# Kernel optimization log

Hardware: AMD Instinct MI355X
Metric: run time of the kernel (lower is better)

The kernel has to match this reference:

```python
import jax, jax.numpy as jnp
import numpy as np

MEM_DIM = 2000
FEA_DIM = 256
SHRINK_THRES = 0.0025
EPS = 1e-06


def setup_inputs() -> dict:
    key = jax.random.key(0)
    k1, k2 = jax.random.split(key)
    x = jax.random.normal(k1, (65536, FEA_DIM), dtype=jnp.float32)
    stdv = 1.0 / np.sqrt(FEA_DIM)
    weight = jax.random.uniform(k2, (MEM_DIM, FEA_DIM), dtype=jnp.float32,
                                minval=-stdv, maxval=stdv)
    temperature = jnp.asarray(0.5, dtype=jnp.float32)
    return {"input": x, "weight": weight, "temperature": temperature}


def hard_shrink_relu(a, lambd=SHRINK_THRES, epsilon=EPS):
    a = jnp.clip(a, -10.0, 10.0)
    denom = jnp.maximum(jnp.abs(a - lambd) + epsilon, epsilon)
    out = jax.nn.relu(a - lambd) * a / denom
    return jnp.where(jnp.isnan(out) | jnp.isinf(out), 0.0, out)


def reference(input, weight, temperature):
    mem_dim = weight.shape[0]
    inv_m = 1.0 / mem_dim
    x = jnp.clip(input, -10.0, 10.0)                      # [N, F]
    att = jnp.einsum('nf,mf->nm', x, weight)              # [N, M]
    att = jax.nn.softmax(att / temperature, axis=1)
    # shrink_thres > 0 branch
    att = hard_shrink_relu(att)
    weight_sum = jnp.sum(att, axis=1, keepdims=True)      # [N, 1]
    zero_mask = weight_sum < 1e-08
    att = att / (weight_sum + 1e-08)
    att = jnp.where(zero_mask, inv_m, att)                # rows with ~zero sum -> uniform
    att = jnp.where(jnp.isnan(att) | jnp.isinf(att), inv_m, att)
    output = jnp.einsum('nm,mf->nf', att, weight)         # [N, F]
    return output, att
```

## Files before the change

kernel.cpp:

```cpp
#include <hip/hip_runtime.h>
#include <hip/hip_bf16.h>
#include <cstdint>

#define N_ROWS 65536
#define FEA    256
#define MEM    2000
#define MEMP   2048
#define LAMBD  0.0025f
#define SEPS   1e-6f
#define NW     16

typedef __attribute__((ext_vector_type(8))) _Float16 f16x8;
typedef __attribute__((ext_vector_type(8))) short    bf16x8;
typedef __attribute__((ext_vector_type(4))) float    f32x4;

__device__ __forceinline__ short f2bf(float f) {
    union { float f; uint32_t u; } v; v.f = f;
    uint32_t r = v.u + 0x7fffu + ((v.u >> 16) & 1u);
    return (short)(r >> 16);
}

__global__ __launch_bounds__(256) void prep_kernel(const float* __restrict__ W,
                                                   _Float16* __restrict__ Whl2,
                                                   short* __restrict__ Wt) {
    __shared__ float tile[8][260];
    const int t  = threadIdx.x;
    const int m0 = blockIdx.x * 8;
    const int row = t >> 5, col = (t & 31) * 8;
    const int m = m0 + row;
    if (m < MEM) {
        f32x4 a = *(const f32x4*)(W + (size_t)m * FEA + col);
        f32x4 b = *(const f32x4*)(W + (size_t)m * FEA + col + 4);
        #pragma unroll
        for (int u = 0; u < 4; ++u) { tile[row][col+u] = a[u]; tile[row][col+4+u] = b[u]; }
    } else {
        #pragma unroll
        for (int u = 0; u < 8; ++u) tile[row][col+u] = 0.f;
    }
    __syncthreads();
    {
        const int c = col >> 5, q = (col >> 3) & 3;
        const int tt = m >> 4, lr = m & 15;
        _Float16 hi[8], lo[8];
        #pragma unroll
        for (int j = 0; j < 8; ++j) {
            float w = tile[row][col + j];
            _Float16 h = (_Float16)w;
            hi[j] = h;
            lo[j] = (_Float16)((w - (float)h) * 2048.0f);
        }
        _Float16* dst = Whl2 + (((size_t)(tt * 8 + c)) << 10) + (q * 16 + lr) * 16;
        *(f16x8*)dst       = *(f16x8*)&hi[0];
        *(f16x8*)(dst + 8) = *(f16x8*)&lo[0];
    }
    {
        short buf[8];
        #pragma unroll
        for (int j = 0; j < 8; ++j) buf[j] = f2bf(tile[j][t]);
        *(bf16x8*)(Wt + (size_t)t * MEMP + m0) = *(bf16x8*)&buf[0];
    }
}

__global__ __launch_bounds__(1024, 4) void score_kernel(const float* __restrict__ x,
                                                        const _Float16* __restrict__ Whl2,
                                                        const float* __restrict__ temp,
                                                        float* __restrict__ att) {
    __shared__ __align__(16) _Float16 ah_s[32][264];
    __shared__ __align__(16) _Float16 al_s[32][264];
    __shared__ float redbuf[NW][32];
    __shared__ float redglob[32];

    const int tid  = threadIdx.x;
    const int lane = tid & 63;
    const int wid  = tid >> 6;
    const int lr   = lane & 15;
    const int q    = lane >> 4;
    const size_t r0 = (size_t)blockIdx.x * 32;
    const float invT = 1.0f / temp[0];

    {
        const int srow = tid >> 5, scol = (tid & 31) * 8;
        const float* xp = x + (r0 + srow) * FEA + scol;
        f32x4 v0 = *(const f32x4*)xp;
        f32x4 v1 = *(const f32x4*)(xp + 4);
        #pragma unroll
        for (int w = 0; w < 4; ++w) {
            float f0 = fminf(fmaxf(v0[w], -10.f), 10.f);
            float f1 = fminf(fmaxf(v1[w], -10.f), 10.f);
            _Float16 h0 = (_Float16)f0, h1 = (_Float16)f1;
            ah_s[srow][scol + w]     = h0;
            ah_s[srow][scol + 4 + w] = h1;
            al_s[srow][scol + w]     = (_Float16)((f0 - (float)h0) * 2048.0f);
            al_s[srow][scol + 4 + w] = (_Float16)((f1 - (float)h1) * 2048.0f);
        }
    }
    __syncthreads();

    f32x4 acc[2][8];
    #pragma unroll
    for (int rg = 0; rg < 2; ++rg)
        #pragma unroll
        for (int jj = 0; jj < 8; ++jj) acc[rg][jj] = (f32x4){0.f, 0.f, 0.f, 0.f};

    #pragma unroll 1
    for (int c = 0; c < 8; ++c) {
        f16x8 ah[2], al[2];
        #pragma unroll
        for (int rg = 0; rg < 2; ++rg) {
            ah[rg] = *(const f16x8*)&ah_s[rg * 16 + lr][c * 32 + q * 8];
            al[rg] = *(const f16x8*)&al_s[rg * 16 + lr][c * 32 + q * 8];
        }
        #pragma unroll
        for (int jj = 0; jj < 8; ++jj) {
            const int t = wid + 16 * jj;
            const _Float16* bp = Whl2 + (((size_t)(t * 8 + c)) << 10) + lane * 16;
            f16x8 bh = *(const f16x8*)bp;
            f16x8 bl = *(const f16x8*)(bp + 8);
            #pragma unroll
            for (int rg = 0; rg < 2; ++rg) {
                f32x4 z = (f32x4){0.f, 0.f, 0.f, 0.f};
                f32x4 t1 = __builtin_amdgcn_mfma_f32_16x16x32_f16(al[rg], bh, z, 0, 0, 0);
                t1 = __builtin_amdgcn_mfma_f32_16x16x32_f16(ah[rg], bl, t1, 0, 0, 0);
                acc[rg][jj] = __builtin_amdgcn_mfma_f32_16x16x32_f16(ah[rg], bh, acc[rg][jj], 0, 0, 0);
                acc[rg][jj] += t1 * (1.0f / 2048.0f);
            }
        }
    }

    const bool lastv = (wid < 13);

    auto xred = [&](float v[2][4], bool ismax) {
        #pragma unroll
        for (int m = 1; m < 16; m <<= 1)
            #pragma unroll
            for (int rg = 0; rg < 2; ++rg)
                #pragma unroll
                for (int i = 0; i < 4; ++i) {
                    float o = __shfl_xor(v[rg][i], m, 64);
                    v[rg][i] = ismax ? fmaxf(v[rg][i], o) : (v[rg][i] + o);
                }
        if (lr == 0) {
            #pragma unroll
            for (int rg = 0; rg < 2; ++rg)
                #pragma unroll
                for (int i = 0; i < 4; ++i) redbuf[wid][rg * 16 + q * 4 + i] = v[rg][i];
        }
        __syncthreads();
        if (tid < 32) {
            float r = redbuf[0][tid];
            #pragma unroll
            for (int w = 1; w < NW; ++w) {
                float o = redbuf[w][tid];
                r = ismax ? fmaxf(r, o) : (r + o);
            }
            redglob[tid] = r;
        }
        __syncthreads();
        #pragma unroll
        for (int rg = 0; rg < 2; ++rg)
            #pragma unroll
            for (int i = 0; i < 4; ++i) v[rg][i] = redglob[rg * 16 + q * 4 + i];
        __syncthreads();
    };

    float M[2][4];
    #pragma unroll
    for (int rg = 0; rg < 2; ++rg)
        #pragma unroll
        for (int i = 0; i < 4; ++i) M[rg][i] = -3.0e38f;
    #pragma unroll
    for (int jj = 0; jj < 8; ++jj) {
        if (jj < 7 || lastv) {
            #pragma unroll
            for (int rg = 0; rg < 2; ++rg)
                #pragma unroll
                for (int i = 0; i < 4; ++i) M[rg][i] = fmaxf(M[rg][i], acc[rg][jj][i]);
        }
    }
    xred(M, true);

    #pragma unroll
    for (int jj = 0; jj < 8; ++jj) {
        const bool v = (jj < 7) || lastv;
        #pragma unroll
        for (int rg = 0; rg < 2; ++rg)
            #pragma unroll
            for (int i = 0; i < 4; ++i)
                acc[rg][jj][i] = v ? __expf((acc[rg][jj][i] - M[rg][i]) * invT) : 0.0f;
    }

    float Z[2][4];
    #pragma unroll
    for (int rg = 0; rg < 2; ++rg)
        #pragma unroll
        for (int i = 0; i < 4; ++i) Z[rg][i] = 0.f;
    #pragma unroll
    for (int jj = 0; jj < 8; ++jj)
        #pragma unroll
        for (int rg = 0; rg < 2; ++rg)
            #pragma unroll
            for (int i = 0; i < 4; ++i) Z[rg][i] += acc[rg][jj][i];
    xred(Z, false);

    #pragma unroll
    for (int rg = 0; rg < 2; ++rg)
        #pragma unroll
        for (int i = 0; i < 4; ++i) Z[rg][i] = 1.0f / Z[rg][i];
    #pragma unroll
    for (int jj = 0; jj < 8; ++jj)
        #pragma unroll
        for (int rg = 0; rg < 2; ++rg)
            #pragma unroll
            for (int i = 0; i < 4; ++i) {
                float a = acc[rg][jj][i] * Z[rg][i];
                float d = a - LAMBD;
                acc[rg][jj][i] = (d > 0.f) ? (d * a) / (d + SEPS) : 0.f;
            }

    float WS[2][4];
    #pragma unroll
    for (int rg = 0; rg < 2; ++rg)
        #pragma unroll
        for (int i = 0; i < 4; ++i) WS[rg][i] = 0.f;
    #pragma unroll
    for (int jj = 0; jj < 8; ++jj)
        #pragma unroll
        for (int rg = 0; rg < 2; ++rg)
            #pragma unroll
            for (int i = 0; i < 4; ++i) WS[rg][i] += acc[rg][jj][i];
    xred(WS, false);

    const float inv_m = 1.0f / (float)MEM;
    float scl[2][4];
    bool  zr[2][4];
    #pragma unroll
    for (int rg = 0; rg < 2; ++rg)
        #pragma unroll
        for (int i = 0; i < 4; ++i) {
            scl[rg][i] = 1.0f / (WS[rg][i] + 1e-8f);
            zr[rg][i]  = (WS[rg][i] < 1e-8f);
        }

    #pragma unroll
    for (int jj = 0; jj < 8; ++jj) {
        if (jj < 7 || lastv) {
            const int mcol = (wid + 16 * jj) * 16 + lr;
            #pragma unroll
            for (int rg = 0; rg < 2; ++rg)
                #pragma unroll
                for (int i = 0; i < 4; ++i) {
                    float vv = zr[rg][i] ? inv_m : acc[rg][jj][i] * scl[rg][i];
                    att[(r0 + rg * 16 + q * 4 + i) * (size_t)MEM + mcol] = vv;
                }
        }
    }
}

__global__ __launch_bounds__(512) void gemm2_kernel(const float* __restrict__ att,
                                                    const short* __restrict__ Wt,
                                                    float* __restrict__ out) {
    __shared__ short Asm[2][128][40];
    __shared__ short Bsm[2][256][40];
    const int tid  = threadIdx.x;
    const int lane = tid & 63;
    const int wid  = tid >> 6;
    const int rg   = wid >> 2;
    const int cg   = wid & 3;
    const int lr   = lane & 15;
    const int lk   = (lane >> 4) * 8;
    const size_t r0 = (size_t)blockIdx.x * 128;

    const int sa_row = tid >> 2, sa_ko = (tid & 3) * 8;
    const int sb_f   = tid >> 1, sb_ko = (tid & 1) * 16;

    auto stage = [&](int buf, int kc) {
        const int k0 = kc * 32;
        {
            int k = k0 + sa_ko;
            short b[8];
            if (k < MEM) {
                const float* ap = att + (r0 + sa_row) * (size_t)MEM + k;
                f32x4 v0 = *(const f32x4*)ap;
                f32x4 v1 = *(const f32x4*)(ap + 4);
                #pragma unroll
                for (int u = 0; u < 4; ++u) { b[u] = f2bf(v0[u]); b[4+u] = f2bf(v1[u]); }
            } else {
                #pragma unroll
                for (int u = 0; u < 8; ++u) b[u] = 0;
            }
            *(bf16x8*)&Asm[buf][sa_row][sa_ko] = *(bf16x8*)&b[0];
        }
        {
            const short* wp = Wt + (size_t)sb_f * MEMP + k0 + sb_ko;
            bf16x8 b0 = *(const bf16x8*)wp;
            bf16x8 b1 = *(const bf16x8*)(wp + 8);
            *(bf16x8*)&Bsm[buf][sb_f][sb_ko]     = b0;
            *(bf16x8*)&Bsm[buf][sb_f][sb_ko + 8] = b1;
        }
    };

    f32x4 acc[4][4];
    #pragma unroll
    for (int i = 0; i < 4; ++i)
        #pragma unroll
        for (int j = 0; j < 4; ++j) acc[i][j] = (f32x4){0.f, 0.f, 0.f, 0.f};

    stage(0, 0);
    int cur = 0;
    for (int kc = 0; kc < 63; ++kc) {
        __syncthreads();
        if (kc + 1 < 63) stage(cur ^ 1, kc + 1);
        bf16x8 a_[4], b_[4];
        #pragma unroll
        for (int i = 0; i < 4; ++i) a_[i] = *(const bf16x8*)&Asm[cur][rg * 64 + i * 16 + lr][lk];
        #pragma unroll
        for (int j = 0; j < 4; ++j) b_[j] = *(const bf16x8*)&Bsm[cur][cg * 64 + j * 16 + lr][lk];
        #pragma unroll
        for (int i = 0; i < 4; ++i)
            #pragma unroll
            for (int j = 0; j < 4; ++j)
                acc[i][j] = __builtin_amdgcn_mfma_f32_16x16x32_bf16(a_[i], b_[j], acc[i][j], 0, 0, 0);
        cur ^= 1;
    }

    #pragma unroll
    for (int i = 0; i < 4; ++i)
        #pragma unroll
        for (int j = 0; j < 4; ++j)
            #pragma unroll
            for (int ii = 0; ii < 4; ++ii) {
                size_t row = r0 + rg * 64 + i * 16 + (lane >> 4) * 4 + ii;
                out[row * FEA + cg * 64 + j * 16 + lr] = acc[i][j][ii];
            }
}

extern "C" void kernel_launch(void* const* d_in, const int* in_sizes, int n_in,
                              void* d_out, int out_size, void* d_ws, size_t ws_size,
                              hipStream_t stream) {
    const float* x = (const float*)d_in[0];
    const float* W = (const float*)d_in[1];
    const float* T = (const float*)d_in[2];
    float* out = (float*)d_out;
    float* att = out + (size_t)N_ROWS * FEA;
    _Float16* Whl2 = (_Float16*)d_ws;
    short*    Wt   = (short*)((char*)d_ws + (2u << 20));

    prep_kernel<<<dim3(256), dim3(256), 0, stream>>>(W, Whl2, Wt);
    score_kernel<<<dim3(N_ROWS / 32), dim3(1024), 0, stream>>>(x, Whl2, T, att);
    gemm2_kernel<<<dim3(N_ROWS / 128), dim3(512), 0, stream>>>(att, Wt, out);
}
```

Baseline: 559.7 us.

## Fold temperature into weights, reorder score MFMA loops, use fast reciprocals

Temperature scaling moves into the weight preparation kernel, so the scores come out already divided by temperature and the softmax subtract-multiply is dropped. The score GEMM loop is swapped to iterate over output tiles outermost with K innermost, keeping separate hi and lo-correction accumulators. This removes the per-step vector add and scale and the zero-init MFMA chain, but LDS A fragments are now reloaded for each tile. Exact divisions are replaced with hardware rcp approximations, and att stores are regrouped by row.

New measurement: 1.289 ms. +130.2%, slower.

```diff
diff --git a/kernel.cpp b/kernel.cpp
--- a/kernel.cpp
+++ b/kernel.cpp
@@ -21,6 +21,7 @@
 }
 
 __global__ __launch_bounds__(256) void prep_kernel(const float* __restrict__ W,
+                                                   const float* __restrict__ temp,
                                                    _Float16* __restrict__ Whl2,
                                                    short* __restrict__ Wt) {
     __shared__ float tile[8][260];
@@ -28,6 +29,7 @@
     const int m0 = blockIdx.x * 8;
     const int row = t >> 5, col = (t & 31) * 8;
     const int m = m0 + row;
+    const float invT = 1.0f / temp[0];
     if (m < MEM) {
         f32x4 a = *(const f32x4*)(W + (size_t)m * FEA + col);
         f32x4 b = *(const f32x4*)(W + (size_t)m * FEA + col + 4);
@@ -44,7 +46,7 @@
         _Float16 hi[8], lo[8];
         #pragma unroll
         for (int j = 0; j < 8; ++j) {
-            float w = tile[row][col + j];
+            float w = tile[row][col + j] * invT;
             _Float16 h = (_Float16)w;
             hi[j] = h;
             lo[j] = (_Float16)((w - (float)h) * 2048.0f);
@@ -63,7 +65,6 @@
 
 __global__ __launch_bounds__(1024, 4) void score_kernel(const float* __restrict__ x,
                                                         const _Float16* __restrict__ Whl2,
-                                                        const float* __restrict__ temp,
                                                         float* __restrict__ att) {
     __shared__ __align__(16) _Float16 ah_s[32][264];
     __shared__ __align__(16) _Float16 al_s[32][264];
@@ -76,7 +77,6 @@
     const int lr   = lane & 15;
     const int q    = lane >> 4;
     const size_t r0 = (size_t)blockIdx.x * 32;
-    const float invT = 1.0f / temp[0];
 
     {
         const int srow = tid >> 5, scol = (tid & 31) * 8;
@@ -97,34 +97,30 @@
     __syncthreads();
 
     f32x4 acc[2][8];
-    #pragma unroll
-    for (int rg = 0; rg < 2; ++rg)
-        #pragma unroll
-        for (int jj = 0; jj < 8; ++jj) acc[rg][jj] = (f32x4){0.f, 0.f, 0.f, 0.f};
 
     #pragma unroll 1
-    for (int c = 0; c < 8; ++c) {
-        f16x8 ah[2], al[2];
-        #pragma unroll
-        for (int rg = 0; rg < 2; ++rg) {
-            ah[rg] = *(const f16x8*)&ah_s[rg * 16 + lr][c * 32 + q * 8];
-            al[rg] = *(const f16x8*)&al_s[rg * 16 + lr][c * 32 + q * 8];
-        }
-        #pragma unroll
-        for (int jj = 0; jj < 8; ++jj) {
-            const int t = wid + 16 * jj;
-            const _Float16* bp = Whl2 + (((size_t)(t * 8 + c)) << 10) + lane * 16;
-            f16x8 bh = *(const f16x8*)bp;
-            f16x8 bl = *(const f16x8*)(bp + 8);
-            #pragma unroll
-            for (int rg = 0; rg < 2; ++rg) {
-                f32x4 z = (f32x4){0.f, 0.f, 0.f, 0.f};
-                f32x4 t1 = __builtin_amdgcn_mfma_f32_16x16x32_f16(al[rg], bh, z, 0, 0, 0);
-                t1 = __builtin_amdgcn_mfma_f32_16x16x32_f16(ah[rg], bl, t1, 0, 0, 0);
-                acc[rg][jj] = __builtin_amdgcn_mfma_f32_16x16x32_f16(ah[rg], bh, acc[rg][jj], 0, 0, 0);
-                acc[rg][jj] += t1 * (1.0f / 2048.0f);
-            }
-        }
+    for (int jj = 0; jj < 8; ++jj) {
+        const int t = wid + 16 * jj;
+        const _Float16* bp = Whl2 + (((size_t)(t * 8)) << 10) + lane * 16;
+        f32x4 zz = (f32x4){0.f, 0.f, 0.f, 0.f};
+        f32x4 hh0 = zz, hh1 = zz, t10 = zz, t11 = zz;
+        #pragma unroll
+        for (int c = 0; c < 8; ++c) {
+            f16x8 bh = *(const f16x8*)(bp + ((size_t)c << 10));
+            f16x8 bl = *(const f16x8*)(bp + ((size_t)c << 10) + 8);
+            f16x8 ah0 = *(const f16x8*)&ah_s[lr]     [c * 32 + q * 8];
+            f16x8 al0 = *(const f16x8*)&al_s[lr]     [c * 32 + q * 8];
+            f16x8 ah1 = *(const f16x8*)&ah_s[16 + lr][c * 32 + q * 8];
+            f16x8 al1 = *(const f16x8*)&al_s[16 + lr][c * 32 + q * 8];
+            hh0 = __builtin_amdgcn_mfma_f32_16x16x32_f16(ah0, bh, hh0, 0, 0, 0);
+            t10 = __builtin_amdgcn_mfma_f32_16x16x32_f16(al0, bh, t10, 0, 0, 0);
+            t10 = __builtin_amdgcn_mfma_f32_16x16x32_f16(ah0, bl, t10, 0, 0, 0);
+            hh1 = __builtin_amdgcn_mfma_f32_16x16x32_f16(ah1, bh, hh1, 0, 0, 0);
+            t11 = __builtin_amdgcn_mfma_f32_16x16x32_f16(al1, bh, t11, 0, 0, 0);
+            t11 = __builtin_amdgcn_mfma_f32_16x16x32_f16(ah1, bl, t11, 0, 0, 0);
+        }
+        acc[0][jj] = hh0 + t10 * (1.0f / 2048.0f);
+        acc[1][jj] = hh1 + t11 * (1.0f / 2048.0f);
     }
 
     const bool lastv = (wid < 13);
@@ -186,7 +182,7 @@
         for (int rg = 0; rg < 2; ++rg)
             #pragma unroll
             for (int i = 0; i < 4; ++i)
-                acc[rg][jj][i] = v ? __expf((acc[rg][jj][i] - M[rg][i]) * invT) : 0.0f;
+                acc[rg][jj][i] = v ? __expf(acc[rg][jj][i] - M[rg][i]) : 0.0f;
     }
 
     float Z[2][4];
@@ -205,7 +201,7 @@
     #pragma unroll
     for (int rg = 0; rg < 2; ++rg)
         #pragma unroll
-        for (int i = 0; i < 4; ++i) Z[rg][i] = 1.0f / Z[rg][i];
+        for (int i = 0; i < 4; ++i) Z[rg][i] = __builtin_amdgcn_rcpf(Z[rg][i]);
     #pragma unroll
     for (int jj = 0; jj < 8; ++jj)
         #pragma unroll
@@ -214,7 +210,8 @@
             for (int i = 0; i < 4; ++i) {
                 float a = acc[rg][jj][i] * Z[rg][i];
                 float d = a - LAMBD;
-                acc[rg][jj][i] = (d > 0.f) ? (d * a) / (d + SEPS) : 0.f;
+                float o = d * a * __builtin_amdgcn_rcpf(d + SEPS);
+                acc[rg][jj][i] = (d > 0.f) ? o : 0.f;
             }
 
     float WS[2][4];
@@ -237,23 +234,23 @@
     for (int rg = 0; rg < 2; ++rg)
         #pragma unroll
         for (int i = 0; i < 4; ++i) {
-            scl[rg][i] = 1.0f / (WS[rg][i] + 1e-8f);
+            scl[rg][i] = __builtin_amdgcn_rcpf(WS[rg][i] + 1e-8f);
             zr[rg][i]  = (WS[rg][i] < 1e-8f);
         }
 
     #pragma unroll
-    for (int jj = 0; jj < 8; ++jj) {
-        if (jj < 7 || lastv) {
-            const int mcol = (wid + 16 * jj) * 16 + lr;
-            #pragma unroll
-            for (int rg = 0; rg < 2; ++rg)
-                #pragma unroll
-                for (int i = 0; i < 4; ++i) {
+    for (int rg = 0; rg < 2; ++rg)
+        #pragma unroll
+        for (int i = 0; i < 4; ++i) {
+            float* p = att + (r0 + rg * 16 + q * 4 + i) * (size_t)MEM + wid * 16 + lr;
+            #pragma unroll
+            for (int jj = 0; jj < 8; ++jj) {
+                if (jj < 7 || lastv) {
                     float vv = zr[rg][i] ? inv_m : acc[rg][jj][i] * scl[rg][i];
-                    att[(r0 + rg * 16 + q * 4 + i) * (size_t)MEM + mcol] = vv;
+                    p[jj * 256] = vv;
                 }
-        }
-    }
+            }
+        }
 }
 
 __global__ __launch_bounds__(512) void gemm2_kernel(const float* __restrict__ att,
@@ -345,7 +342,7 @@
     _Float16* Whl2 = (_Float16*)d_ws;
     short*    Wt   = (short*)((char*)d_ws + (2u << 20));
 
-    prep_kernel<<<dim3(256), dim3(256), 0, stream>>>(W, Whl2, Wt);
-    score_kernel<<<dim3(N_ROWS / 32), dim3(1024), 0, stream>>>(x, Whl2, T, att);
+    prep_kernel<<<dim3(256), dim3(256), 0, stream>>>(W, T, Whl2, Wt);
+    score_kernel<<<dim3(N_ROWS / 32), dim3(1024), 0, stream>>>(x, Whl2, att);
     gemm2_kernel<<<dim3(N_ROWS / 128), dim3(512), 0, stream>>>(att, Wt, out);
 }
```
